# Performance work log

Measured on AMD Instinct MI355X. Metric: run time of the kernel, lower is better.

Reference implementation:

```python
import jax, jax.numpy as jnp
import numpy as np

B, S, H, NH = 2, 2048, 1024, 16
HD = H // NH  # head_size = 64


def setup_inputs() -> dict:
    key = jax.random.key(0)
    ks = jax.random.split(key, 9)
    sc = 0.02
    return {
        "hidden_states": jax.random.normal(ks[0], (B, S, H), dtype=jnp.float32),
        "Wq": jax.random.normal(ks[1], (H, H), dtype=jnp.float32) * sc,
        "bq": jax.random.normal(ks[2], (H,), dtype=jnp.float32) * sc,
        "Wk": jax.random.normal(ks[3], (H, H), dtype=jnp.float32) * sc,
        "bk": jax.random.normal(ks[4], (H,), dtype=jnp.float32) * sc,
        "Wv": jax.random.normal(ks[5], (H, H), dtype=jnp.float32) * sc,
        "bv": jax.random.normal(ks[6], (H,), dtype=jnp.float32) * sc,
        "Wo": jax.random.normal(ks[7], (H, H), dtype=jnp.float32) * sc,
        "bo": jax.random.normal(ks[8], (H,), dtype=jnp.float32) * sc,
    }


def reference(hidden_states, Wq, bq, Wk, bk, Wv, bv, Wo, bo):
    b, s, h = hidden_states.shape
    # nn.Linear: y = x @ W.T + b
    q = hidden_states @ Wq.T + bq
    k = hidden_states @ Wk.T + bk
    v = hidden_states @ Wv.T + bv
    q = q.reshape(b, s, NH, HD)
    k = k.reshape(b, s, NH, HD)
    v = v.reshape(b, s, NH, HD)
    # scores: [b, heads, q, k]
    scores = jnp.einsum("bqhd,bkhd->bhqk", q, k) / jnp.sqrt(jnp.float32(HD))
    # causal mask: triu(ones, diagonal=1) positions set to -inf
    causal = jnp.triu(jnp.ones((s, s), dtype=bool), k=1)
    scores = jnp.where(causal[None, None], -jnp.inf, scores)
    attn = jax.nn.softmax(scores, axis=-1)
    ctx = jnp.einsum("bhqk,bkhd->bqhd", attn, v).reshape(b, s, h)
    return ctx @ Wo.T + bo
```

## Files before the change

### kernel.cpp

```cpp
#include <hip/hip_runtime.h>
#include <hip/hip_bf16.h>

#define B_  2
#define S_  2048
#define H_  1024
#define NH_ 16
#define HD_ 64
#define SMAX_ 12.0f

typedef unsigned short u16;
typedef unsigned int   u32;
typedef __attribute__((ext_vector_type(4)))  float  f32x4;
typedef __attribute__((ext_vector_type(16))) float  f32x16;
typedef __attribute__((ext_vector_type(8)))  __bf16 bf16x8;
typedef __attribute__((ext_vector_type(4)))  unsigned int u32x4;
typedef __attribute__((ext_vector_type(4)))  unsigned short u16x4;

__device__ __forceinline__ u16 f2bf(float f) {
  unsigned u = __builtin_bit_cast(unsigned, f);
  u += 0x7fffu + ((u >> 16) & 1u);
  return (u16)(u >> 16);
}
__device__ __forceinline__ u32 cvtpk(float lo, float hi) {
  u32 r;
  asm("v_cvt_pk_bf16_f32 %0, %1, %2" : "=v"(r) : "v"(lo), "v"(hi));
  return r;
}
__device__ __forceinline__ float ex2(float x) {
  float r;
  asm("v_exp_f32 %0, %1" : "=v"(r) : "v"(x));
  return r;
}

__device__ __forceinline__ void gload_lds16(const void* g, void* l) {
  __builtin_amdgcn_global_load_lds(
      (const __attribute__((address_space(1))) void*)g,
      (__attribute__((address_space(3))) void*)l, 16, 0, 0);
}

#define NX_ (4u * 1024u * 1024u)
__global__ __launch_bounds__(256) void cvt_all(const float* __restrict__ x,
                                               const float* __restrict__ w0, const float* __restrict__ w1,
                                               const float* __restrict__ w2, const float* __restrict__ w3,
                                               u16* __restrict__ xb,
                                               u16* __restrict__ o0, u16* __restrict__ o1,
                                               u16* __restrict__ o2, u16* __restrict__ o3) {
  size_t i4 = ((size_t)blockIdx.x * 256 + threadIdx.x) * 4;
  const float* src; u16* dst; size_t off;
  if (i4 < (size_t)NX_) { src = x; dst = xb; off = i4; }
  else {
    size_t j = i4 - NX_;
    int seg = (int)(j >> 20);
    off = j & ((1u << 20) - 1);
    src = seg == 0 ? w0 : seg == 1 ? w1 : seg == 2 ? w2 : w3;
    dst = seg == 0 ? o0 : seg == 1 ? o1 : seg == 2 ? o2 : o3;
  }
  float4 v = *reinterpret_cast<const float4*>(src + off);
  u16x4 o;
  o[0] = f2bf(v.x); o[1] = f2bf(v.y); o[2] = f2bf(v.z); o[3] = f2bf(v.w);
  *reinterpret_cast<u16x4*>(dst + off) = o;
}

__device__ __forceinline__ void store_out(float* C, size_t idx, float v) { C[idx] = v; }
__device__ __forceinline__ void store_out(u16* C, size_t idx, float v) { C[idx] = f2bf(v); }

template <int MI, typename OutT>
__device__ __forceinline__ void gemm_core(const u16* __restrict__ A, const u16* __restrict__ Bw,
                                          const float* __restrict__ bias, OutT* __restrict__ C,
                                          int M, int N, int K, float oscale, int m0, int n0,
                                          u16* lsA, u16* lsB) {
  const int t = threadIdx.x;
  const int w = t >> 6, lane = t & 63;
  const int g = lane >> 4, c = lane & 15;
  const int wr = w >> 1, wc = w & 1;

  f32x4 acc[MI][4] = {};
  const int rowS = w * 16 + (lane >> 2);
  const int sgr  = (lane & 3) ^ ((lane >> 2) & 3) ^ ((lane >> 4) & 3);
  const int colS = sgr * 8;
  const int rcol = (g ^ (c & 3) ^ ((c >> 2) & 3)) * 8;

  for (int k0 = 0; k0 < K; k0 += 32) {
    __syncthreads();
#pragma unroll
    for (int r = 0; r < MI / 2; ++r)
      gload_lds16(A + (size_t)(m0 + r * 64 + rowS) * K + k0 + colS, lsA + r * 2048 + w * 512);
#pragma unroll
    for (int r = 0; r < 2; ++r)
      gload_lds16(Bw + (size_t)(n0 + r * 64 + rowS) * K + k0 + colS, lsB + r * 2048 + w * 512);
    asm volatile("s_waitcnt vmcnt(0)" ::: "memory");
    __syncthreads();

    bf16x8 af[MI], bfr[4];
#pragma unroll
    for (int mi = 0; mi < MI; ++mi)
      af[mi] = *reinterpret_cast<const bf16x8*>(&lsA[(wr * (MI * 16) + mi * 16 + c) * 32 + rcol]);
#pragma unroll
    for (int ni = 0; ni < 4; ++ni)
      bfr[ni] = *reinterpret_cast<const bf16x8*>(&lsB[(wc * 64 + ni * 16 + c) * 32 + rcol]);
#pragma unroll
    for (int mi = 0; mi < MI; ++mi)
#pragma unroll
      for (int ni = 0; ni < 4; ++ni)
        acc[mi][ni] = __builtin_amdgcn_mfma_f32_16x16x32_bf16(af[mi], bfr[ni], acc[mi][ni], 0, 0, 0);
  }

#pragma unroll
  for (int mi = 0; mi < MI; ++mi) {
    int rowb = m0 + wr * (MI * 16) + mi * 16 + g * 4;
#pragma unroll
    for (int ni = 0; ni < 4; ++ni) {
      int col = n0 + wc * 64 + ni * 16 + c;
      float bv = bias[col];
#pragma unroll
      for (int r = 0; r < 4; ++r) {
        float v = (acc[mi][ni][r] + bv) * oscale;
        store_out(C, (size_t)(rowb + r) * N + col, v);
      }
    }
  }
}

__global__ __launch_bounds__(256) void gemm_qkv(const u16* __restrict__ xb,
                                                const u16* __restrict__ Wq, const u16* __restrict__ Wk,
                                                const u16* __restrict__ Wv,
                                                const float* __restrict__ bq, const float* __restrict__ bk,
                                                const float* __restrict__ bv,
                                                u16* __restrict__ Q, u16* __restrict__ Kb, u16* __restrict__ Vb,
                                                int M, int K, float qscale) {
  __shared__ u16 lsA[4096];
  __shared__ u16 lsB[4096];
  const int fid = blockIdx.x;
  const int xcd = fid & 7, i = fid >> 3;
  const int mloc = i / 24, nn = i % 24;
  const int m0 = (xcd * 4 + mloc) * 128;
  const int ng = nn * 128;
  const int sel = ng >> 10, n0 = ng & 1023;
  const u16*  W    = sel == 0 ? Wq : sel == 1 ? Wk : Wv;
  const float* bia = sel == 0 ? bq : sel == 1 ? bk : bv;
  u16*        Cp   = sel == 0 ? Q  : sel == 1 ? Kb : Vb;
  float os = sel == 0 ? qscale : 1.0f;
  gemm_core<4, u16>(xb, W, bia, Cp, M, 1024, K, os, m0, n0, lsA, lsB);
}

__global__ __launch_bounds__(256) void gemm_wo(const u16* __restrict__ A, const u16* __restrict__ Bw,
                                               const float* __restrict__ bias, float* __restrict__ C,
                                               int M, int N, int K) {
  __shared__ u16 lsA[2048];
  __shared__ u16 lsB[4096];
  const int fid = blockIdx.x;
  const int xcd = fid & 7, i = fid >> 3;
  const int mloc = i >> 3, nn = i & 7;
  const int m0 = (xcd * 8 + mloc) * 64;
  const int n0 = nn * 128;
  gemm_core<2, float>(A, Bw, bias, C, M, N, K, 1.0f, m0, n0, lsA, lsB);
}

__global__ __launch_bounds__(256, 4) void attn_fwd(const u16* __restrict__ Qg,
                                                   const u16* __restrict__ Kg,
                                                   const u16* __restrict__ Vg,
                                                   u16* __restrict__ Og) {
  __shared__ __align__(16) u16 smem[18432];
  u16* lsKb = smem;
  u16* lsVb = smem + 8192;
  float* lsO  = (float*)smem;
  float* lsML = (float*)((char*)smem + 20480);
  u16*   lsOT = smem + 10752;

  const int blk = blockIdx.x;
  const int xcd = blk & 7, i = blk >> 3;
  const int pj = i & 15, bgrp = i >> 4;
  const int bh = xcd * 4 + bgrp;
  const int h = bh & 15, b = bh >> 4;

  const int t = threadIdx.x, w = t >> 6, lane = t & 63;
  const int c5 = lane & 31, hi = lane >> 5;
  const int sub = w & 1, par = w >> 1;
  const size_t headoff = (size_t)b * (S_ * H_) + (size_t)h * HD_;

  const int sp = w & 1, sh = w >> 1;
  const int kRowLoc = 16 * sh + (lane >> 3);
  const int kSrcCol = ((lane & 7) ^ (lane >> 3)) << 4;
  const int vKvLoc  = 16 * sh + 2 * (lane >> 3);
  const int vD0     = 8 * (lane & 7);
  const int vKvx    = vKvLoc ^ (((lane & 7) & 3) << 3);

  int qkOff[4];
#pragma unroll
  for (int kc = 0; kc < 4; ++kc)
    qkOff[kc] = c5 * 128 + ((32 * kc + 16 * hi) ^ ((c5 & 7) << 4));
  const int pvRow0 = c5 * 80, pvRow1 = (32 + c5) * 80;
  int pvCol[2];
#pragma unroll
  for (int kp2 = 0; kp2 < 2; ++kp2)
    pvCol[kp2] = 2 * ((16 * kp2 + 8 * hi) ^ ((c5 >> 3) << 3));

  u32x4 vA, vB;
  auto STAGE = [&](int m) {
    const int kv0 = m * 64 + 32 * sp;
    const u16* vp = Vg + headoff + (size_t)(kv0 + vKvLoc) * H_ + vD0;
    vA = *reinterpret_cast<const u32x4*>(vp);
    vB = *reinterpret_cast<const u32x4*>(vp + H_);
    char* kt = (char*)(lsKb + ((m & 1) * 2 + sp) * 2048) + 16 * sh * 128;
    const char* ks = (const char*)(Kg + headoff + (size_t)(kv0 + kRowLoc) * H_) + kSrcCol;
    gload_lds16(ks, kt);
    gload_lds16(ks + 8 * (H_ * 2), kt + 8 * 128);
  };
  auto WRITEVT = [&](int m) {
    u16* vt = lsVb + ((m & 1) * 2 + sp) * 2560;
#pragma unroll
    for (int jj = 0; jj < 4; ++jj) {
      u32 lo  = __builtin_amdgcn_perm(vB[jj], vA[jj], 0x05040100u);
      u32 hi2 = __builtin_amdgcn_perm(vB[jj], vA[jj], 0x07060302u);
      *reinterpret_cast<u32*>(vt + (vD0 + 2 * jj) * 40 + vKvx)     = lo;
      *reinterpret_cast<u32*>(vt + (vD0 + 2 * jj + 1) * 40 + vKvx) = hi2;
    }
  };

  for (int seg = 0; seg < 2; ++seg) {
    const int qt = seg ? pj : 31 - pj;
    const int q0w = qt * 64 + 32 * sub;
    if (seg) __syncthreads();

    bf16x8 aq[4];
#pragma unroll
    for (int kc = 0; kc < 4; ++kc)
      aq[kc] = *reinterpret_cast<const bf16x8*>(Qg + headoff + (size_t)(q0w + c5) * H_ + kc * 16 + hi * 8);

    f32x16 o0 = {}, o1 = {};
    float lrun = 0.f;

    STAGE(0);
    asm volatile("s_waitcnt vmcnt(2)" ::: "memory");
    WRITEVT(0);
    asm volatile("s_waitcnt lgkmcnt(0)" ::: "memory");
    asm volatile("s_waitcnt vmcnt(0)" ::: "memory");
    __builtin_amdgcn_s_barrier();

    for (int n = 0; n <= qt; ++n) {
      const int buf = n & 1;
      const bool st = n < qt;
      if (st) STAGE(n + 1);

      const bool live = (2 * n + par) <= (2 * qt + sub);
      const bool diag = (2 * n + par) == (2 * qt + sub);
      f32x16 sc = {};
      if (live) {
        const char* kb = (const char*)(lsKb + (buf * 2 + par) * 2048);
        __builtin_amdgcn_s_setprio(1);
#pragma unroll
        for (int kc = 0; kc < 4; ++kc) {
          bf16x8 ak = *reinterpret_cast<const bf16x8*>(kb + qkOff[kc]);
          sc = __builtin_amdgcn_mfma_f32_32x32x16_bf16(ak, aq[kc], sc, 0, 0, 0);
        }
        __builtin_amdgcn_s_setprio(0);
        if (diag) {
#pragma unroll
          for (int r = 0; r < 16; ++r) {
            int kvl = (r & 3) + 8 * (r >> 2) + 4 * hi;
            sc[r] = (kvl > c5) ? -1e30f : sc[r];
          }
        }
      }

      if (st) {
        asm volatile("s_waitcnt vmcnt(2)" ::: "memory");
        WRITEVT(n + 1);
      }

      if (live) {
        const char* vtb = (const char*)(lsVb + (buf * 2 + par) * 2560);
        float rs = 0.f;
        u32 wd0[2], wd1[2], wd2[2], wd3[2];
#pragma unroll
        for (int a = 0; a < 4; ++a) {
          float p0 = ex2(sc[4 * a + 0] - SMAX_), p1 = ex2(sc[4 * a + 1] - SMAX_);
          float p2 = ex2(sc[4 * a + 2] - SMAX_), p3 = ex2(sc[4 * a + 3] - SMAX_);
          rs += (p0 + p1) + (p2 + p3);
          u32* wdp = a == 0 ? wd0 : a == 1 ? wd1 : a == 2 ? wd2 : wd3;
          wdp[0] = cvtpk(p0, p1);
          wdp[1] = cvtpk(p2, p3);
        }
        lrun += rs;
        __builtin_amdgcn_s_setprio(1);
#pragma unroll
        for (int kp2 = 0; kp2 < 2; ++kp2) {
          u32 wa0 = kp2 ? wd2[0] : wd0[0], wa1 = kp2 ? wd2[1] : wd0[1];
          u32 wb0 = kp2 ? wd3[0] : wd1[0], wb1 = kp2 ? wd3[1] : wd1[1];
          u32 own0 = hi ? wb0 : wa0, own1 = hi ? wb1 : wa1;
          u32 snd0 = hi ? wa0 : wb0, snd1 = hi ? wa1 : wb1;
          u32 oth0 = (u32)__shfl_xor((int)snd0, 32);
          u32 oth1 = (u32)__shfl_xor((int)snd1, 32);
          u32x4 pw;
          pw[0] = hi ? oth0 : own0;
          pw[1] = hi ? oth1 : own1;
          pw[2] = hi ? own0 : oth0;
          pw[3] = hi ? own1 : oth1;
          bf16x8 pb = __builtin_bit_cast(bf16x8, pw);
          bf16x8 av0 = *reinterpret_cast<const bf16x8*>(vtb + pvRow0 + pvCol[kp2]);
          bf16x8 av1 = *reinterpret_cast<const bf16x8*>(vtb + pvRow1 + pvCol[kp2]);
          o0 = __builtin_amdgcn_mfma_f32_32x32x16_bf16(av0, pb, o0, 0, 0, 0);
          o1 = __builtin_amdgcn_mfma_f32_32x32x16_bf16(av1, pb, o1, 0, 0, 0);
        }
        __builtin_amdgcn_s_setprio(0);
      }

      asm volatile("s_waitcnt lgkmcnt(0)" ::: "memory");
      if (st) asm volatile("s_waitcnt vmcnt(0)" ::: "memory");
      __builtin_amdgcn_s_barrier();
    }

    lrun += (float)__shfl_xor(lrun, 32);

    if (par == 0) {
      if (hi == 0) lsML[sub * 32 + c5] = lrun;
#pragma unroll
      for (int dt = 0; dt < 2; ++dt) {
        float* dst = lsO + ((size_t)((sub * 2 + dt) * 64 + lane)) * 20;
        const f32x16& oo = dt ? o1 : o0;
#pragma unroll
        for (int k4 = 0; k4 < 4; ++k4) {
          f32x4 v4 = {oo[4 * k4], oo[4 * k4 + 1], oo[4 * k4 + 2], oo[4 * k4 + 3]};
          *reinterpret_cast<f32x4*>(dst + 4 * k4) = v4;
        }
      }
    }
    __syncthreads();
    if (par == 1) {
      float lA = lsML[sub * 32 + c5];
      float linv = 1.0f / (lA + lrun);
      u16* ot = lsOT + sub * 2304;
#pragma unroll
      for (int dt = 0; dt < 2; ++dt) {
        const float* sp2 = lsO + ((size_t)((sub * 2 + dt) * 64 + lane)) * 20;
        f32x4 a4[4];
#pragma unroll
        for (int k4 = 0; k4 < 4; ++k4) a4[k4] = *reinterpret_cast<const f32x4*>(sp2 + 4 * k4);
        const f32x16& oo = dt ? o1 : o0;
#pragma unroll
        for (int a = 0; a < 4; ++a)
#pragma unroll
          for (int u = 0; u < 2; ++u) {
            int r = 4 * a + 2 * u;
            float e0 = (a4[a][2 * u]     + oo[r])     * linv;
            float e1 = (a4[a][2 * u + 1] + oo[r + 1]) * linv;
            int d = 32 * dt + 8 * a + 4 * hi + 2 * u;
            *reinterpret_cast<u32*>(ot + c5 * 72 + d) = cvtpk(e0, e1);
          }
      }
      asm volatile("s_waitcnt lgkmcnt(0)" ::: "memory");
      __builtin_amdgcn_sched_barrier(0);
#pragma unroll
      for (int rr = 0; rr < 4; ++rr) {
        int q = 8 * rr + (lane >> 3);
        int d8 = (lane & 7) * 8;
        u32x4 vv = *reinterpret_cast<const u32x4*>(lsOT + sub * 2304 + q * 72 + d8);
        *reinterpret_cast<u32x4*>(Og + headoff + (size_t)(qt * 64 + 32 * sub + q) * H_ + d8) = vv;
      }
    }
  }
}

extern "C" void kernel_launch(void* const* d_in, const int* in_sizes, int n_in,
                              void* d_out, int out_size, void* d_ws, size_t ws_size,
                              hipStream_t stream) {
  const float* x  = (const float*)d_in[0];
  const float* Wq = (const float*)d_in[1];
  const float* bq = (const float*)d_in[2];
  const float* Wk = (const float*)d_in[3];
  const float* bk = (const float*)d_in[4];
  const float* Wv = (const float*)d_in[5];
  const float* bv = (const float*)d_in[6];
  const float* Wo = (const float*)d_in[7];
  const float* bo = (const float*)d_in[8];
  float* out = (float*)d_out;

  const size_t MT = (size_t)B_ * S_;
  char* p = (char*)d_ws;
  u16* xb  = (u16*)p; p += MT * H_ * 2;
  u16* Wqb = (u16*)p; p += (size_t)H_ * H_ * 2;
  u16* Wkb = (u16*)p; p += (size_t)H_ * H_ * 2;
  u16* Wvb = (u16*)p; p += (size_t)H_ * H_ * 2;
  u16* Wob = (u16*)p; p += (size_t)H_ * H_ * 2;
  u16* Qb  = (u16*)p; p += MT * H_ * 2;
  u16* Kb  = (u16*)p; p += MT * H_ * 2;
  u16* Vb  = (u16*)p; p += MT * H_ * 2;
  u16* Cb  = xb;

  cvt_all<<<8192, 256, 0, stream>>>(x, Wq, Wk, Wv, Wo, xb, Wqb, Wkb, Wvb, Wob);

  const float qscale = 0.125f * 1.44269504088896f;
  gemm_qkv<<<768, 256, 0, stream>>>(xb, Wqb, Wkb, Wvb, bq, bk, bv,
                                    Qb, Kb, Vb, (int)MT, H_, qscale);

  attn_fwd<<<512, 256, 0, stream>>>(Qb, Kb, Vb, Cb);

  gemm_wo<<<512, 256, 0, stream>>>(Cb, Wob, bo, out, (int)MT, H_, H_);
}
```

Before: 106.6 us.

## Double GEMM K-step per barrier and use permlane32 swap in attention P exchange

The GEMM main loop now loads two 32-wide K slices per iteration into doubled LDS buffers. This halves the number of barrier and vmcnt waits per tile and issues more MFMAs between synchronisations. Separately, the attention kernel replaces the shfl_xor-based exchange of packed P values across wave halves with v_permlane32_swap_b32 instructions, which avoids ds_bpermute traffic and select logic. The cost is higher LDS use in the GEMM kernels, which may reduce occupancy.

```diff
diff --git a/kernel.cpp b/kernel.cpp
--- a/kernel.cpp
+++ b/kernel.cpp
@@ -80,29 +80,40 @@
   const int colS = sgr * 8;
   const int rcol = (g ^ (c & 3) ^ ((c >> 2) & 3)) * 8;
 
-  for (int k0 = 0; k0 < K; k0 += 32) {
+  for (int k0 = 0; k0 < K; k0 += 64) {
     __syncthreads();
 #pragma unroll
-    for (int r = 0; r < MI / 2; ++r)
-      gload_lds16(A + (size_t)(m0 + r * 64 + rowS) * K + k0 + colS, lsA + r * 2048 + w * 512);
-#pragma unroll
-    for (int r = 0; r < 2; ++r)
-      gload_lds16(Bw + (size_t)(n0 + r * 64 + rowS) * K + k0 + colS, lsB + r * 2048 + w * 512);
+    for (int half = 0; half < 2; ++half) {
+      const int kh0 = k0 + half * 32;
+#pragma unroll
+      for (int r = 0; r < MI / 2; ++r)
+        gload_lds16(A + (size_t)(m0 + r * 64 + rowS) * K + kh0 + colS,
+                    lsA + half * (MI * 1024) + r * 2048 + w * 512);
+#pragma unroll
+      for (int r = 0; r < 2; ++r)
+        gload_lds16(Bw + (size_t)(n0 + r * 64 + rowS) * K + kh0 + colS,
+                    lsB + half * 4096 + r * 2048 + w * 512);
+    }
     asm volatile("s_waitcnt vmcnt(0)" ::: "memory");
     __syncthreads();
 
-    bf16x8 af[MI], bfr[4];
-#pragma unroll
-    for (int mi = 0; mi < MI; ++mi)
-      af[mi] = *reinterpret_cast<const bf16x8*>(&lsA[(wr * (MI * 16) + mi * 16 + c) * 32 + rcol]);
-#pragma unroll
-    for (int ni = 0; ni < 4; ++ni)
-      bfr[ni] = *reinterpret_cast<const bf16x8*>(&lsB[(wc * 64 + ni * 16 + c) * 32 + rcol]);
-#pragma unroll
-    for (int mi = 0; mi < MI; ++mi)
+#pragma unroll
+    for (int half = 0; half < 2; ++half) {
+      const u16* la = lsA + half * (MI * 1024);
+      const u16* lb = lsB + half * 4096;
+      bf16x8 af[MI], bfr[4];
+#pragma unroll
+      for (int mi = 0; mi < MI; ++mi)
+        af[mi] = *reinterpret_cast<const bf16x8*>(&la[(wr * (MI * 16) + mi * 16 + c) * 32 + rcol]);
 #pragma unroll
       for (int ni = 0; ni < 4; ++ni)
-        acc[mi][ni] = __builtin_amdgcn_mfma_f32_16x16x32_bf16(af[mi], bfr[ni], acc[mi][ni], 0, 0, 0);
+        bfr[ni] = *reinterpret_cast<const bf16x8*>(&lb[(wc * 64 + ni * 16 + c) * 32 + rcol]);
+#pragma unroll
+      for (int mi = 0; mi < MI; ++mi)
+#pragma unroll
+        for (int ni = 0; ni < 4; ++ni)
+          acc[mi][ni] = __builtin_amdgcn_mfma_f32_16x16x32_bf16(af[mi], bfr[ni], acc[mi][ni], 0, 0, 0);
+    }
   }
 
 #pragma unroll
@@ -128,8 +139,8 @@
                                                 const float* __restrict__ bv,
                                                 u16* __restrict__ Q, u16* __restrict__ Kb, u16* __restrict__ Vb,
                                                 int M, int K, float qscale) {
-  __shared__ u16 lsA[4096];
-  __shared__ u16 lsB[4096];
+  __shared__ u16 lsA[2 * 4096];
+  __shared__ u16 lsB[2 * 4096];
   const int fid = blockIdx.x;
   const int xcd = fid & 7, i = fid >> 3;
   const int mloc = i / 24, nn = i % 24;
@@ -146,8 +157,8 @@
 __global__ __launch_bounds__(256) void gemm_wo(const u16* __restrict__ A, const u16* __restrict__ Bw,
                                                const float* __restrict__ bias, float* __restrict__ C,
                                                int M, int N, int K) {
-  __shared__ u16 lsA[2048];
-  __shared__ u16 lsB[4096];
+  __shared__ u16 lsA[2 * 2048];
+  __shared__ u16 lsB[2 * 4096];
   const int fid = blockIdx.x;
   const int xcd = fid & 7, i = fid >> 3;
   const int mloc = i >> 3, nn = i & 7;
@@ -285,17 +296,11 @@
         __builtin_amdgcn_s_setprio(1);
 #pragma unroll
         for (int kp2 = 0; kp2 < 2; ++kp2) {
-          u32 wa0 = kp2 ? wd2[0] : wd0[0], wa1 = kp2 ? wd2[1] : wd0[1];
-          u32 wb0 = kp2 ? wd3[0] : wd1[0], wb1 = kp2 ? wd3[1] : wd1[1];
-          u32 own0 = hi ? wb0 : wa0, own1 = hi ? wb1 : wa1;
-          u32 snd0 = hi ? wa0 : wb0, snd1 = hi ? wa1 : wb1;
-          u32 oth0 = (u32)__shfl_xor((int)snd0, 32);
-          u32 oth1 = (u32)__shfl_xor((int)snd1, 32);
-          u32x4 pw;
-          pw[0] = hi ? oth0 : own0;
-          pw[1] = hi ? oth1 : own1;
-          pw[2] = hi ? own0 : oth0;
-          pw[3] = hi ? own1 : oth1;
+          u32 A0 = kp2 ? wd2[0] : wd0[0], A1 = kp2 ? wd2[1] : wd0[1];
+          u32 B0 = kp2 ? wd3[0] : wd1[0], B1 = kp2 ? wd3[1] : wd1[1];
+          asm("v_permlane32_swap_b32 %0, %1" : "+v"(A0), "+v"(B0));
+          asm("v_permlane32_swap_b32 %0, %1" : "+v"(A1), "+v"(B1));
+          u32x4 pw = {A0, A1, B0, B1};
           bf16x8 pb = __builtin_bit_cast(bf16x8, pw);
           bf16x8 av0 = *reinterpret_cast<const bf16x8*>(vtb + pvRow0 + pvCol[kp2]);
           bf16x8 av1 = *reinterpret_cast<const bf16x8*>(vtb + pvRow1 + pvCol[kp2]);
```

After: 111.6 us. 4.7% more time.
